# Performance work log

Measured on AMD Instinct MI355X. Metric: run time of the kernel, lower is better.

The kernel has to match this reference:

```python
import jax, jax.numpy as jnp
import numpy as np

N_LAT, N_LON = 121, 240
N = N_LAT * N_LON          # 29040 nodes (fixed by module's reshape)
DEG = 16
E = N * DEG                # 464640 edges
H = 128                    # input_nf = output_nf = hidden_nf
LV = 11                    # pressure levels (coord_mlp outputs 11*2)
EDGE_IN = 2 * H + 34       # source + target + w_diff(33) + edge_attr(1)


def setup_inputs() -> dict:
    key = jax.random.key(0)
    ks = jax.random.split(key, 18)
    def w(k, shape, s=0.05):
        return jax.random.normal(k, shape, dtype=jnp.float32) * s
    return {
        'h': w(ks[0], (N, H), 1.0),
        'u': w(ks[1], (N, LV), 1.0),
        'v': w(ks[2], (N, LV), 1.0),
        'edge_attr': w(ks[3], (E, 1), 1.0),
        # edge MLP: Linear(EDGE_IN,H) ReLU Linear(H,H) ReLU
        'W_e1': w(ks[4], (EDGE_IN, H)), 'b_e1': jnp.zeros((H,), jnp.float32),
        'W_e2': w(ks[5], (H, H)),       'b_e2': jnp.zeros((H,), jnp.float32),
        # node MLP: Linear(2H+H,H) ReLU Linear(H,H)
        'W_n1': w(ks[6], (3 * H, H)),   'b_n1': jnp.zeros((H,), jnp.float32),
        'W_n2': w(ks[7], (H, H)),       'b_n2': jnp.zeros((H,), jnp.float32),
        # coord MLP: Linear(H,H) ReLU Linear(H,22,bias=False) with tiny xavier gain
        'W_c1': w(ks[8], (H, H)),       'b_c1': jnp.zeros((H,), jnp.float32),
        'W_cl': w(ks[9], (H, 2 * LV), 0.001),
        'edge_index': jax.random.randint(ks[10], (2, E), 0, N, dtype=jnp.int32),
    }


def reference(h, u, v, edge_attr,
              W_e1, b_e1, W_e2, b_e2,
              W_n1, b_n1, W_n2, b_n2,
              W_c1, b_c1, W_cl,
              edge_index):
    row, col = edge_index[0], edge_index[1]

    # ---- coord2radial ----
    uc, vc = u[col], v[col]          # [E, LV]
    ur, vr = u[row], v[row]
    col_speed = jnp.sqrt(uc * uc + vc * vc)
    row_speed = jnp.sqrt(ur * ur + vr * vr)
    rel_dirt = (uc * ur + vc * vr) / (col_speed * row_speed)
    w_diff = jnp.concatenate([rel_dirt, col_speed, row_speed], axis=1)  # [E, 33]

    # ---- edge model ----
    edge_in = jnp.concatenate([h[row], h[col], w_diff, edge_attr], axis=1)  # [E, EDGE_IN]
    edge_feat = jax.nn.relu(jax.nn.relu(edge_in @ W_e1 + b_e1) @ W_e2 + b_e2)  # [E, H]

    # ---- node model (scatter-sum + lat-band mean pooling) ----
    agg = jax.ops.segment_sum(edge_feat, row, num_segments=N)  # [N, H]
    lat = agg.reshape(N_LAT, N_LON, H).mean(axis=1, keepdims=True)  # [121,1,H]
    lat_agg = jnp.broadcast_to(lat, (N_LAT, N_LON, H)).reshape(N, H)
    node_in = jnp.concatenate([h, agg, lat_agg], axis=1)  # [N, 3H]
    h_out = jax.nn.relu(node_in @ W_n1 + b_n1) @ W_n2 + b_n2 + h  # residual

    # ---- coord model (scatter-mean with clamp) ----
    ef = (jax.nn.relu(edge_feat @ W_c1 + b_c1) @ W_cl).reshape(E, 2, LV)
    radial = jnp.stack([uc, vc], axis=1)                 # [E, 2, LV]
    rad2 = jnp.sqrt(jnp.sum(radial * radial, axis=-1))   # [E, 2] (per-component magnitude)
    wind = ef * rad2[:, :, None]                         # [E, 2, LV]
    cnt = jnp.maximum(
        jax.ops.segment_sum(jnp.ones((E,), jnp.float32), row, num_segments=N), 1.0)[:, None]
    agg_u = jnp.clip(jax.ops.segment_sum(wind[:, 0, :], row, num_segments=N) / cnt, -100.0, 100.0)
    agg_v = jnp.clip(jax.ops.segment_sum(wind[:, 1, :], row, num_segments=N) / cnt, -100.0, 100.0)

    return h_out, agg_u, agg_v
```

## Files before the change

### kernel.cpp

```cpp
#include <hip/hip_runtime.h>
#include <hip/hip_bf16.h>
#include <math.h>

#define NN   29040
#define NLAT 121
#define NLON 240
#define HD   128
#define LVN  11
#define EE   464640

typedef __attribute__((ext_vector_type(8))) short short8;
typedef __attribute__((ext_vector_type(4))) float f4;

#define OFF_WE1 0
#define OFF_WE2 40960
#define OFF_WC1 57344
#define OFF_WCL 73728
#define OFF_WN1 77824
#define OFF_WN2 126976
#define WP_SHORTS 143360

__device__ inline short f2b(float x) {
    union { __hip_bfloat16 b; short s; } v;
    v.b = __float2bfloat16(x);
    return v.s;
}
__device__ inline float b2f(unsigned short b) {
    union { unsigned u; float f; } v; v.u = ((unsigned)b) << 16;
    return v.f;
}

#define SB_HIST  1815
#define SB_HCAST 1815
#define SB_UV    114
#define SB_WP    70

__global__ __launch_bounds__(256)
void setup_kernel(const int* __restrict__ eidx, int* __restrict__ cnt,
                  const float* __restrict__ h, short* __restrict__ hb,
                  const float* __restrict__ u, const float* __restrict__ v,
                  float* __restrict__ uvrec,
                  const float* __restrict__ We1, const float* __restrict__ We2,
                  const float* __restrict__ Wc1, const float* __restrict__ Wcl,
                  const float* __restrict__ Wn1, const float* __restrict__ Wn2,
                  short* __restrict__ wp)
{
    const int b = blockIdx.x, tid = threadIdx.x;
    if (b < SB_HIST) {
        int e = b * 256 + tid;
        atomicAdd(&cnt[eidx[e]], 1);
        return;
    }
    if (b < SB_HIST + SB_HCAST) {
        int idx = (b - SB_HIST) * 256 + tid;
        const float4* hf = (const float4*)h;
        float4 a = hf[idx * 2], c = hf[idx * 2 + 1];
        short8 o;
        o[0] = f2b(a.x); o[1] = f2b(a.y); o[2] = f2b(a.z); o[3] = f2b(a.w);
        o[4] = f2b(c.x); o[5] = f2b(c.y); o[6] = f2b(c.z); o[7] = f2b(c.w);
        ((short8*)hb)[idx] = o;
        return;
    }
    if (b < SB_HIST + SB_HCAST + SB_UV) {
        int n = (b - SB_HIST - SB_HCAST) * 256 + tid;
        if (n >= NN) return;
        float* r = uvrec + (size_t)n * 36;
        float un = 0.f, vn = 0.f;
#pragma unroll
        for (int l = 0; l < LVN; ++l) {
            float uu = u[n * LVN + l], vv = v[n * LVN + l];
            float s = sqrtf(uu * uu + vv * vv);
            r[l]      = uu / s;
            r[11 + l] = vv / s;
            r[22 + l] = s;
            un += uu * uu; vn += vv * vv;
        }
        r[33] = sqrtf(un);
        r[34] = sqrtf(vn);
        r[35] = 0.f;
        return;
    }
    {
        int fg = (b - SB_HIST - SB_HCAST - SB_UV) * 4 + (tid >> 6);
        const int l = tid & 63;
        int kind, f, base;
        if (fg < 80)       { kind = 0; f = fg;       base = OFF_WE1; }
        else if (fg < 112) { kind = 1; f = fg - 80;  base = OFF_WE2; }
        else if (fg < 144) { kind = 2; f = fg - 112; base = OFF_WC1; }
        else if (fg < 152) { kind = 3; f = fg - 144; base = OFF_WCL; }
        else if (fg < 248) { kind = 4; f = fg - 152; base = OFF_WN1; }
        else               { kind = 5; f = fg - 248; base = OFF_WN2; }
        const int nfw = (kind == 3) ? 2 : 8;
        const int kf = f / nfw, nf = f % nfw;
        short* dst = wp + base + (size_t)f * 512 + l * 8;
        for (int i = 0; i < 8; ++i) {
            int k = kf * 32 + ((l >> 4) << 3) + i;
            int n = nf * 16 + (l & 15);
            float val = 0.f;
            if (kind == 0) {
                int r = (k < 33) ? (256 + k) : (k == 33 ? 289 : (k < 64 ? -1 : k - 64));
                if (r >= 0) val = We1[r * HD + n];
            } else if (kind == 1) val = We2[k * HD + n];
            else if (kind == 2)  val = Wc1[k * HD + n];
            else if (kind == 3)  { if (n < 22) val = Wcl[k * 22 + n]; }
            else if (kind == 4)  val = Wn1[k * HD + n];
            else                 val = Wn2[k * HD + n];
            dst[i] = f2b(val);
        }
    }
}

__global__ __launch_bounds__(1024)
void scan_kernel(const int* __restrict__ cnt, int* __restrict__ off)
{
    __shared__ int part[1024];
    const int tid = threadIdx.x;
    const int CH = 29;
    int lo = tid * CH, hi = min(lo + CH, NN);
    int s = 0;
    for (int i = lo; i < hi; ++i) s += cnt[i];
    part[tid] = s;
    __syncthreads();
    for (int d = 1; d < 1024; d <<= 1) {
        int vv = (tid >= d) ? part[tid - d] : 0;
        __syncthreads();
        part[tid] += vv;
        __syncthreads();
    }
    int run = (tid == 0) ? 0 : part[tid - 1];
    for (int i = lo; i < hi; ++i) { off[i] = run; run += cnt[i]; }
    if (tid == 1023) off[NN] = run;
}

__global__ __launch_bounds__(256)
void scatter_kernel(const int* __restrict__ eidx, const int* __restrict__ off,
                    int* __restrict__ cur, int* __restrict__ csr)
{
    int e = blockIdx.x * 256 + threadIdx.x;
    if (e >= EE) return;
    int row = eidx[e];
    int p = atomicAdd(&cur[row], 1);
    csr[off[row] + p] = e;
}

template<int KF, int NF>
__device__ inline void layer_gemm(const short* At, int rs, const short* Wp,
                                  const float* bias, f4* acc, int w, int lane)
{
    const int m = 16 * w + (lane & 15);
    const char* arow = (const char*)At + m * rs;
    const int sw = (m & 7) << 4;
    const int kb = (lane >> 4) << 4;
#pragma unroll
    for (int nf = 0; nf < NF; ++nf) {
        float bv = bias ? bias[nf * 16 + (lane & 15)] : 0.f;
        acc[nf] = (f4){bv, bv, bv, bv};
    }
#pragma unroll
    for (int kf = 0; kf < KF; ++kf) {
        short8 a = *(const short8*)(arow + ((kf * 64 + kb) ^ sw));
        const short8* wr = (const short8*)(Wp + (size_t)kf * NF * 512) + lane;
#pragma unroll
        for (int nf = 0; nf < NF; ++nf) {
            short8 bfr = wr[nf * 64];
            acc[nf] = __builtin_amdgcn_mfma_f32_16x16x32_bf16(a, bfr, acc[nf], 0, 0, 0);
        }
    }
}

template<int NF>
__device__ inline void store_tile(short* tile, int rs, const f4* acc, int w, int lane)
{
    const int rb = 16 * w + ((lane >> 4) << 2);
    const int cb = (lane & 15) * 2;
#pragma unroll
    for (int nf = 0; nf < NF; ++nf)
#pragma unroll
        for (int r = 0; r < 4; ++r) {
            int row = rb + r;
            float vv = fmaxf(acc[nf][r], 0.f);
            *(short*)((char*)tile + row * rs + ((cb + nf * 32) ^ ((row & 7) << 4))) = f2b(vv);
        }
}

__global__ __launch_bounds__(256, 4)
void edge_mfma(const short* __restrict__ hb, const float* __restrict__ uvrec,
               const float* __restrict__ ea,
               const float* __restrict__ be1, const float* __restrict__ be2,
               const float* __restrict__ bc1,
               const short* __restrict__ wp,
               const int* __restrict__ eidx, const int* __restrict__ csr,
               float* __restrict__ agg, float* __restrict__ aggu,
               float* __restrict__ aggv)
{
    __shared__ short Twd[64 * 64];
    __shared__ short T1[64 * 128];
    __shared__ int   rows_s[64];
    __shared__ float radu_s[64], radv_s[64];

    const int tid = threadIdx.x, lane = tid & 63, w = tid >> 6;
    const int e0 = blockIdx.x * 64;
    const int mrow = 16 * w + (lane & 15);
    const int koff = 8 * (lane >> 4);
    const int sw   = (mrow & 7) << 4;

    int e1 = csr[e0 + mrow];
    int rowm = eidx[e1], colm = eidx[EE + e1];
    short8 ar[4], ac[4];
    {
        const short* hr = hb + (size_t)rowm * HD + koff;
        const short* hc = hb + (size_t)colm * HD + koff;
#pragma unroll
        for (int kf = 0; kf < 4; ++kf) {
            ar[kf] = *(const short8*)(hr + kf * 32);
            ac[kf] = *(const short8*)(hc + kf * 32);
        }
    }

    {
        const int m2 = tid >> 2, q = tid & 3;
        const int sw2 = (m2 & 7) << 4;
        int e2 = csr[e0 + m2];
        int row2 = eidx[e2], col2 = eidx[EE + e2];
        const float* rc = uvrec + (size_t)col2 * 36;
        const float* rr = uvrec + (size_t)row2 * 36;
        char* arow = (char*)(Twd + m2 * 64);
        short8 z = {0, 0, 0, 0, 0, 0, 0, 0};
        *(short8*)(arow + q * 32) = z;
        *(short8*)(arow + q * 32 + 16) = z;
        for (int l = q; l < LVN; l += 4) {
            float rel = rc[l] * rr[l] + rc[11 + l] * rr[11 + l];
            *(short*)(arow + ((2 * l) ^ sw2))        = f2b(rel);
            *(short*)(arow + ((2 * (11 + l)) ^ sw2)) = f2b(rc[22 + l]);
            *(short*)(arow + ((2 * (22 + l)) ^ sw2)) = f2b(rr[22 + l]);
        }
        if (q == 0) { rows_s[m2] = row2; radu_s[m2] = rc[33]; radv_s[m2] = rc[34]; }
        if (q == 3) *(short*)(arow + ((2 * 33) ^ sw2)) = f2b(ea[e2]);
    }
    __syncthreads();

    f4 acc[8];
#pragma unroll
    for (int nf = 0; nf < 8; ++nf) {
        float bv = be1[nf * 16 + (lane & 15)];
        acc[nf] = (f4){bv, bv, bv, bv};
    }
    {
        const char* awd = (const char*)(Twd + mrow * 64);
#pragma unroll
        for (int kf = 0; kf < 2; ++kf) {
            short8 a = *(const short8*)(awd + ((kf * 64 + 2 * koff) ^ sw));
            const short8* wr = (const short8*)(wp + OFF_WE1 + (size_t)kf * 8 * 512) + lane;
#pragma unroll
            for (int nf = 0; nf < 8; ++nf)
                acc[nf] = __builtin_amdgcn_mfma_f32_16x16x32_bf16(a, wr[nf * 64], acc[nf], 0, 0, 0);
        }
#pragma unroll
        for (int kf = 0; kf < 4; ++kf) {
            const short8* wr = (const short8*)(wp + OFF_WE1 + (size_t)(kf + 2) * 8 * 512) + lane;
#pragma unroll
            for (int nf = 0; nf < 8; ++nf)
                acc[nf] = __builtin_amdgcn_mfma_f32_16x16x32_bf16(ar[kf], wr[nf * 64], acc[nf], 0, 0, 0);
        }
#pragma unroll
        for (int kf = 0; kf < 4; ++kf) {
            const short8* wr = (const short8*)(wp + OFF_WE1 + (size_t)(kf + 6) * 8 * 512) + lane;
#pragma unroll
            for (int nf = 0; nf < 8; ++nf)
                acc[nf] = __builtin_amdgcn_mfma_f32_16x16x32_bf16(ac[kf], wr[nf * 64], acc[nf], 0, 0, 0);
        }
    }
    store_tile<8>(T1, 256, acc, w, lane);

    layer_gemm<4, 8>(T1, 256, wp + OFF_WE2, be2, acc, w, lane);
    store_tile<8>(T1, 256, acc, w, lane);

    f4 accC[8];
    layer_gemm<4, 8>(T1, 256, wp + OFF_WC1, bc1, accC, w, lane);

    __syncthreads();
    {
        const int n = tid & 127, qq = tid >> 7;
        const int m0 = qq * 32;
        int curr = rows_s[m0]; float s = 0.f;
        for (int m = m0; m < m0 + 32; ++m) {
            int r = rows_s[m];
            float vv = b2f(*(const unsigned short*)((const char*)(T1 + m * 128) + ((2 * n) ^ ((m & 7) << 4))));
            if (r != curr) { atomicAdd(&agg[(size_t)curr * HD + n], s); s = 0.f; curr = r; }
            s += vv;
        }
        atomicAdd(&agg[(size_t)curr * HD + n], s);
    }
    __syncthreads();

    store_tile<8>(T1, 256, accC, w, lane);
    layer_gemm<4, 2>(T1, 256, wp + OFF_WCL, (const float*)nullptr, accC, w, lane);
    float* O22 = (float*)Twd;
    {
        const int rb = 16 * w + ((lane >> 4) << 2), cb = lane & 15;
#pragma unroll
        for (int nf = 0; nf < 2; ++nf)
#pragma unroll
            for (int r = 0; r < 4; ++r)
                O22[(rb + r) * 32 + nf * 16 + cb] = accC[nf][r];
    }
    __syncthreads();

    {
        const int c = tid & 31, qq = tid >> 5;
        if (c < 22) {
            const bool isU = c < LVN;
            const int lvl = isU ? c : c - LVN;
            float* dst = isU ? aggu : aggv;
            const float* radp = isU ? radu_s : radv_s;
            const int m0 = qq * 8;
            int curr = rows_s[m0]; float s = 0.f;
            for (int m = m0; m < m0 + 8; ++m) {
                int r = rows_s[m];
                float vv = O22[m * 32 + c] * radp[m];
                if (r != curr) { atomicAdd(&dst[(size_t)curr * LVN + lvl], s); s = 0.f; curr = r; }
                s += vv;
            }
            atomicAdd(&dst[(size_t)curr * LVN + lvl], s);
        }
    }
}

__global__ __launch_bounds__(256)
void post_kernel(const float* __restrict__ agg, short* __restrict__ latb,
                 float* __restrict__ aggu, float* __restrict__ aggv,
                 const int* __restrict__ off)
{
    const int b = blockIdx.x, tid = threadIdx.x;
    if (b < NLAT) {
        __shared__ float part[256];
        const int j = tid & 127, half = tid >> 7;
        float s = 0.f;
        for (int lon = half * 120; lon < (half + 1) * 120; ++lon)
            s += agg[((size_t)b * NLON + lon) * HD + j];
        part[tid] = s;
        __syncthreads();
        if (tid < 128)
            latb[(size_t)b * HD + tid] = f2b((part[tid] + part[128 + tid]) * (1.0f / NLON));
        return;
    }
    int tt = (b - NLAT) * 256 + tid;
    if (tt >= NN * LVN) return;
    int n = tt / LVN;
    float c = fmaxf((float)(off[n + 1] - off[n]), 1.f);
    float xu = aggu[tt] / c, xv = aggv[tt] / c;
    aggu[tt] = fminf(fmaxf(xu, -100.f), 100.f);
    aggv[tt] = fminf(fmaxf(xv, -100.f), 100.f);
}

__global__ __launch_bounds__(512, 4)
void node_mfma(const short* __restrict__ hb, const float* __restrict__ h,
               const short* __restrict__ latb,
               const float* __restrict__ bn1, const float* __restrict__ bn2,
               const short* __restrict__ wp, float* __restrict__ out)
{
    __shared__ short T1[128 * 128];
    const int tid = threadIdx.x, lane = tid & 63, w = tid >> 6;
    const int n0 = blockIdx.x * 128;
    const int mrow = 16 * w + (lane & 15);
    const int koff = 8 * (lane >> 4);
    const int n = n0 + mrow;
    const int nc = (n < NN) ? n : (NN - 1);
    const short* hp = hb + (size_t)nc * HD + koff;
    const float* ap = out + (size_t)nc * HD + koff;
    const short* lp = latb + (size_t)(nc / NLON) * HD + koff;

    f4 acc[8];
#pragma unroll
    for (int nf = 0; nf < 8; ++nf) {
        float bv = bn1[nf * 16 + (lane & 15)];
        acc[nf] = (f4){bv, bv, bv, bv};
    }
#pragma unroll
    for (int kf = 0; kf < 4; ++kf) {
        short8 a = *(const short8*)(hp + kf * 32);
        const short8* wr = (const short8*)(wp + OFF_WN1 + (size_t)kf * 8 * 512) + lane;
#pragma unroll
        for (int nf = 0; nf < 8; ++nf)
            acc[nf] = __builtin_amdgcn_mfma_f32_16x16x32_bf16(a, wr[nf * 64], acc[nf], 0, 0, 0);
    }
#pragma unroll
    for (int kf = 0; kf < 4; ++kf) {
        short8 a;
#pragma unroll
        for (int j = 0; j < 8; ++j) a[j] = f2b(ap[kf * 32 + j]);
        const short8* wr = (const short8*)(wp + OFF_WN1 + (size_t)(kf + 4) * 8 * 512) + lane;
#pragma unroll
        for (int nf = 0; nf < 8; ++nf)
            acc[nf] = __builtin_amdgcn_mfma_f32_16x16x32_bf16(a, wr[nf * 64], acc[nf], 0, 0, 0);
    }
#pragma unroll
    for (int kf = 0; kf < 4; ++kf) {
        short8 a = *(const short8*)(lp + kf * 32);
        const short8* wr = (const short8*)(wp + OFF_WN1 + (size_t)(kf + 8) * 8 * 512) + lane;
#pragma unroll
        for (int nf = 0; nf < 8; ++nf)
            acc[nf] = __builtin_amdgcn_mfma_f32_16x16x32_bf16(a, wr[nf * 64], acc[nf], 0, 0, 0);
    }
    store_tile<8>(T1, 256, acc, w, lane);
    layer_gemm<4, 8>(T1, 256, wp + OFF_WN2, bn2, acc, w, lane);

    const int rb = 16 * w + ((lane >> 4) << 2), cb = lane & 15;
#pragma unroll
    for (int nf = 0; nf < 8; ++nf)
#pragma unroll
        for (int r = 0; r < 4; ++r) {
            int gn = n0 + rb + r;
            if (gn < NN) {
                int colj = nf * 16 + cb;
                out[(size_t)gn * HD + colj] = acc[nf][r] + h[(size_t)gn * HD + colj];
            }
        }
}

extern "C" void kernel_launch(void* const* d_in, const int* in_sizes, int n_in,
                              void* d_out, int out_size, void* d_ws, size_t ws_size,
                              hipStream_t stream)
{
    const float* h   = (const float*)d_in[0];
    const float* u   = (const float*)d_in[1];
    const float* v   = (const float*)d_in[2];
    const float* ea  = (const float*)d_in[3];
    const float* We1 = (const float*)d_in[4];
    const float* be1 = (const float*)d_in[5];
    const float* We2 = (const float*)d_in[6];
    const float* be2 = (const float*)d_in[7];
    const float* Wn1 = (const float*)d_in[8];
    const float* bn1 = (const float*)d_in[9];
    const float* Wn2 = (const float*)d_in[10];
    const float* bn2 = (const float*)d_in[11];
    const float* Wc1 = (const float*)d_in[12];
    const float* bc1 = (const float*)d_in[13];
    const float* Wcl = (const float*)d_in[14];
    const int*   eidx = (const int*)d_in[15];

    float* out  = (float*)d_out;
    float* agg  = out;
    float* aggu = out + (size_t)NN * HD;
    float* aggv = aggu + (size_t)NN * LVN;

    char* p = (char*)d_ws;
    short* wp  = (short*)p;                  p += (size_t)WP_SHORTS * 2;
    int*   off = (int*)p;                    p += (size_t)(NN + 1) * 4;
    int*   csr = (int*)p;                    p += (size_t)EE * 4;
    p = (char*)(((size_t)p + 15) & ~(size_t)15);
    short* hb  = (short*)p;                  p += (size_t)NN * HD * 2;
    float* uvr = (float*)p;                  p += (size_t)NN * 36 * 4;
    short* latb = (short*)p;                 p += (size_t)NLAT * HD * 2;
    p = (char*)(((size_t)p + 15) & ~(size_t)15);
    int*   cnt = (int*)p;                    p += (size_t)NN * 4;
    int*   cur = (int*)p;

    hipMemsetAsync(d_out, 0, (size_t)out_size * sizeof(float), stream);
    hipMemsetAsync(cnt, 0, (size_t)2 * NN * sizeof(int), stream);

    setup_kernel<<<SB_HIST + SB_HCAST + SB_UV + SB_WP, 256, 0, stream>>>(
        eidx, cnt, h, hb, u, v, uvr, We1, We2, Wc1, Wcl, Wn1, Wn2, wp);
    scan_kernel<<<1, 1024, 0, stream>>>(cnt, off);
    scatter_kernel<<<EE / 256, 256, 0, stream>>>(eidx, off, cur, csr);

    edge_mfma<<<EE / 64, 256, 0, stream>>>(hb, uvr, ea, be1, be2, bc1,
                                           wp, eidx, csr, agg, aggu, aggv);

    post_kernel<<<NLAT + (NN * LVN + 255) / 256, 256, 0, stream>>>(
        agg, latb, aggu, aggv, off);

    node_mfma<<<(NN + 127) / 128, 512, 0, stream>>>(hb, h, latb, bn1, bn2, wp, agg);
}
```

Baseline: 345.0 us.

## Switch edge and node MLPs to 32x32x16 MFMA with 2x2 wave tiling

Replaces the 16x16x32 bf16 MFMA tiling, where each wave owned 16 rows and all 128 columns, with 32x32x16 MFMA tiles. Waves are now arranged as row-groups by column-halves, so each wave computes a 32x64 sub-tile. Packed weights are re-laid out for the new B-fragment shape. Gathered h rows are loaded per k-step instead of being prefetched into registers, and extra __syncthreads are added because waves now share LDS tiles across column halves. The intent is higher MFMA efficiency and fewer weight loads per output. In exchange the coord-head GEMM runs on only half the waves, and the added barriers and unprefetched gathers may stall.

Result: faster. 294.6 us (-14.6%).

```diff
diff --git a/kernel.cpp b/kernel.cpp
--- a/kernel.cpp
+++ b/kernel.cpp
@@ -10,7 +10,7 @@
 #define EE   464640
 
 typedef __attribute__((ext_vector_type(8))) short short8;
-typedef __attribute__((ext_vector_type(4))) float f4;
+typedef __attribute__((ext_vector_type(16))) float f16v;
 
 #define OFF_WE1 0
 #define OFF_WE2 40960
@@ -90,12 +90,12 @@
         else if (fg < 152) { kind = 3; f = fg - 144; base = OFF_WCL; }
         else if (fg < 248) { kind = 4; f = fg - 152; base = OFF_WN1; }
         else               { kind = 5; f = fg - 248; base = OFF_WN2; }
-        const int nfw = (kind == 3) ? 2 : 8;
+        const int nfw = (kind == 3) ? 1 : 4;
         const int kf = f / nfw, nf = f % nfw;
         short* dst = wp + base + (size_t)f * 512 + l * 8;
         for (int i = 0; i < 8; ++i) {
-            int k = kf * 32 + ((l >> 4) << 3) + i;
-            int n = nf * 16 + (l & 15);
+            int k = kf * 16 + ((l >> 5) << 3) + i;
+            int n = nf * 32 + (l & 31);
             float val = 0.f;
             if (kind == 0) {
                 int r = (k < 33) ? (256 + k) : (k == 33 ? 289 : (k < 64 ? -1 : k - 64));
@@ -143,43 +143,43 @@
     csr[off[row] + p] = e;
 }
 
-template<int KF, int NF>
-__device__ inline void layer_gemm(const short* At, int rs, const short* Wp,
-                                  const float* bias, f4* acc, int w, int lane)
-{
-    const int m = 16 * w + (lane & 15);
-    const char* arow = (const char*)At + m * rs;
-    const int sw = (m & 7) << 4;
-    const int kb = (lane >> 4) << 4;
-#pragma unroll
-    for (int nf = 0; nf < NF; ++nf) {
-        float bv = bias ? bias[nf * 16 + (lane & 15)] : 0.f;
-        acc[nf] = (f4){bv, bv, bv, bv};
+template<int KF, int NFL, int NJ>
+__device__ inline void gemm32_lds(const short* At, const short* Wp, int nf0,
+                                  const float* bias, f16v* acc,
+                                  int mrow, int colbase, int r31, int kh, int lane)
+{
+    const char* arow = (const char*)At + mrow * 256;
+    const int sw = (mrow & 7) << 4;
+#pragma unroll
+    for (int j = 0; j < NJ; ++j) {
+        float bv = bias ? bias[colbase + j * 32 + r31] : 0.f;
+#pragma unroll
+        for (int q = 0; q < 16; ++q) acc[j][q] = bv;
     }
 #pragma unroll
     for (int kf = 0; kf < KF; ++kf) {
-        short8 a = *(const short8*)(arow + ((kf * 64 + kb) ^ sw));
-        const short8* wr = (const short8*)(Wp + (size_t)kf * NF * 512) + lane;
-#pragma unroll
-        for (int nf = 0; nf < NF; ++nf) {
-            short8 bfr = wr[nf * 64];
-            acc[nf] = __builtin_amdgcn_mfma_f32_16x16x32_bf16(a, bfr, acc[nf], 0, 0, 0);
-        }
-    }
-}
-
-template<int NF>
-__device__ inline void store_tile(short* tile, int rs, const f4* acc, int w, int lane)
-{
-    const int rb = 16 * w + ((lane >> 4) << 2);
-    const int cb = (lane & 15) * 2;
-#pragma unroll
-    for (int nf = 0; nf < NF; ++nf)
-#pragma unroll
-        for (int r = 0; r < 4; ++r) {
-            int row = rb + r;
-            float vv = fmaxf(acc[nf][r], 0.f);
-            *(short*)((char*)tile + row * rs + ((cb + nf * 32) ^ ((row & 7) << 4))) = f2b(vv);
+        short8 a = *(const short8*)(arow + ((kf * 32 + 16 * kh) ^ sw));
+#pragma unroll
+        for (int j = 0; j < NJ; ++j) {
+            short8 bfr = *(const short8*)(Wp + (size_t)(kf * NFL + nf0 + j) * 512 + lane * 8);
+            acc[j] = __builtin_amdgcn_mfma_f32_32x32x16_bf16(a, bfr, acc[j], 0, 0, 0);
+        }
+    }
+}
+
+template<int NJ>
+__device__ inline void store32(short* tile, const f16v* acc, int rg, int colbase,
+                               int r31, int kh, bool relu)
+{
+#pragma unroll
+    for (int j = 0; j < NJ; ++j)
+#pragma unroll
+        for (int reg = 0; reg < 16; ++reg) {
+            int row = rg * 32 + (reg & 3) + 8 * (reg >> 2) + 4 * kh;
+            int cb2 = (colbase + j * 32 + r31) * 2;
+            float vv = acc[j][reg];
+            if (relu) vv = fmaxf(vv, 0.f);
+            *(short*)((char*)tile + row * 256 + (cb2 ^ ((row & 7) << 4))) = f2b(vv);
         }
 }
 
@@ -199,23 +199,17 @@
     __shared__ float radu_s[64], radv_s[64];
 
     const int tid = threadIdx.x, lane = tid & 63, w = tid >> 6;
+    const int rg = w >> 1, cg = w & 1;
     const int e0 = blockIdx.x * 64;
-    const int mrow = 16 * w + (lane & 15);
-    const int koff = 8 * (lane >> 4);
-    const int sw   = (mrow & 7) << 4;
+    const int r31 = lane & 31, kh = lane >> 5;
+    const int mrow = rg * 32 + r31;
+    const int sw = (mrow & 7) << 4;
+    const int colbase = cg * 64;
 
     int e1 = csr[e0 + mrow];
     int rowm = eidx[e1], colm = eidx[EE + e1];
-    short8 ar[4], ac[4];
-    {
-        const short* hr = hb + (size_t)rowm * HD + koff;
-        const short* hc = hb + (size_t)colm * HD + koff;
-#pragma unroll
-        for (int kf = 0; kf < 4; ++kf) {
-            ar[kf] = *(const short8*)(hr + kf * 32);
-            ac[kf] = *(const short8*)(hc + kf * 32);
-        }
-    }
+    const short* hr = hb + (size_t)rowm * HD + 8 * kh;
+    const short* hc = hb + (size_t)colm * HD + 8 * kh;
 
     {
         const int m2 = tid >> 2, q = tid & 3;
@@ -239,83 +233,87 @@
     }
     __syncthreads();
 
-    f4 acc[8];
-#pragma unroll
-    for (int nf = 0; nf < 8; ++nf) {
-        float bv = be1[nf * 16 + (lane & 15)];
-        acc[nf] = (f4){bv, bv, bv, bv};
+    f16v acc[2];
+#pragma unroll
+    for (int j = 0; j < 2; ++j) {
+        float bv = be1[colbase + j * 32 + r31];
+#pragma unroll
+        for (int q = 0; q < 16; ++q) acc[j][q] = bv;
     }
     {
         const char* awd = (const char*)(Twd + mrow * 64);
 #pragma unroll
-        for (int kf = 0; kf < 2; ++kf) {
-            short8 a = *(const short8*)(awd + ((kf * 64 + 2 * koff) ^ sw));
-            const short8* wr = (const short8*)(wp + OFF_WE1 + (size_t)kf * 8 * 512) + lane;
-#pragma unroll
-            for (int nf = 0; nf < 8; ++nf)
-                acc[nf] = __builtin_amdgcn_mfma_f32_16x16x32_bf16(a, wr[nf * 64], acc[nf], 0, 0, 0);
-        }
-#pragma unroll
         for (int kf = 0; kf < 4; ++kf) {
-            const short8* wr = (const short8*)(wp + OFF_WE1 + (size_t)(kf + 2) * 8 * 512) + lane;
-#pragma unroll
-            for (int nf = 0; nf < 8; ++nf)
-                acc[nf] = __builtin_amdgcn_mfma_f32_16x16x32_bf16(ar[kf], wr[nf * 64], acc[nf], 0, 0, 0);
-        }
-#pragma unroll
-        for (int kf = 0; kf < 4; ++kf) {
-            const short8* wr = (const short8*)(wp + OFF_WE1 + (size_t)(kf + 6) * 8 * 512) + lane;
-#pragma unroll
-            for (int nf = 0; nf < 8; ++nf)
-                acc[nf] = __builtin_amdgcn_mfma_f32_16x16x32_bf16(ac[kf], wr[nf * 64], acc[nf], 0, 0, 0);
-        }
-    }
-    store_tile<8>(T1, 256, acc, w, lane);
-
-    layer_gemm<4, 8>(T1, 256, wp + OFF_WE2, be2, acc, w, lane);
-    store_tile<8>(T1, 256, acc, w, lane);
-
-    f4 accC[8];
-    layer_gemm<4, 8>(T1, 256, wp + OFF_WC1, bc1, accC, w, lane);
-
-    __syncthreads();
+            short8 a = *(const short8*)(awd + ((kf * 32 + 16 * kh) ^ sw));
+#pragma unroll
+            for (int j = 0; j < 2; ++j) {
+                short8 bfr = *(const short8*)(wp + OFF_WE1 + (size_t)(kf * 4 + cg * 2 + j) * 512 + lane * 8);
+                acc[j] = __builtin_amdgcn_mfma_f32_32x32x16_bf16(a, bfr, acc[j], 0, 0, 0);
+            }
+        }
+#pragma unroll
+        for (int s = 0; s < 8; ++s) {
+            short8 a = *(const short8*)(hr + s * 16);
+#pragma unroll
+            for (int j = 0; j < 2; ++j) {
+                short8 bfr = *(const short8*)(wp + OFF_WE1 + (size_t)((s + 4) * 4 + cg * 2 + j) * 512 + lane * 8);
+                acc[j] = __builtin_amdgcn_mfma_f32_32x32x16_bf16(a, bfr, acc[j], 0, 0, 0);
+            }
+        }
+#pragma unroll
+        for (int s = 0; s < 8; ++s) {
+            short8 a = *(const short8*)(hc + s * 16);
+#pragma unroll
+            for (int j = 0; j < 2; ++j) {
+                short8 bfr = *(const short8*)(wp + OFF_WE1 + (size_t)((s + 12) * 4 + cg * 2 + j) * 512 + lane * 8);
+                acc[j] = __builtin_amdgcn_mfma_f32_32x32x16_bf16(a, bfr, acc[j], 0, 0, 0);
+            }
+        }
+    }
+    store32<2>(T1, acc, rg, colbase, r31, kh, true);
+    __syncthreads();
+
+    gemm32_lds<8, 4, 2>(T1, wp + OFF_WE2, cg * 2, be2, acc, mrow, colbase, r31, kh, lane);
+    __syncthreads();
+    store32<2>(T1, acc, rg, colbase, r31, kh, true);
+    __syncthreads();
+
+    gemm32_lds<8, 4, 2>(T1, wp + OFF_WC1, cg * 2, bc1, acc, mrow, colbase, r31, kh, lane);
+
     {
-        const int n = tid & 127, qq = tid >> 7;
-        const int m0 = qq * 32;
-        int curr = rows_s[m0]; float s = 0.f;
+        const int col = colbase + lane;
+        const int m0 = rg * 32;
+        int curr = rows_s[m0];
+        float s = 0.f;
         for (int m = m0; m < m0 + 32; ++m) {
             int r = rows_s[m];
-            float vv = b2f(*(const unsigned short*)((const char*)(T1 + m * 128) + ((2 * n) ^ ((m & 7) << 4))));
-            if (r != curr) { atomicAdd(&agg[(size_t)curr * HD + n], s); s = 0.f; curr = r; }
+            float vv = b2f(*(const unsigned short*)((const char*)T1 + m * 256 + (((col & 127) * 2) ^ ((m & 7) << 4))));
+            if (r != curr) { atomicAdd(&agg[(size_t)curr * HD + (col & 127)], s); s = 0.f; curr = r; }
             s += vv;
         }
-        atomicAdd(&agg[(size_t)curr * HD + n], s);
-    }
-    __syncthreads();
-
-    store_tile<8>(T1, 256, accC, w, lane);
-    layer_gemm<4, 2>(T1, 256, wp + OFF_WCL, (const float*)nullptr, accC, w, lane);
-    float* O22 = (float*)Twd;
-    {
-        const int rb = 16 * w + ((lane >> 4) << 2), cb = lane & 15;
-#pragma unroll
-        for (int nf = 0; nf < 2; ++nf)
-#pragma unroll
-            for (int r = 0; r < 4; ++r)
-                O22[(rb + r) * 32 + nf * 16 + cb] = accC[nf][r];
-    }
-    __syncthreads();
-
-    {
-        const int c = tid & 31, qq = tid >> 5;
+        atomicAdd(&agg[(size_t)curr * HD + (col & 127)], s);
+    }
+    __syncthreads();
+    store32<2>(T1, acc, rg, colbase, r31, kh, true);
+    __syncthreads();
+
+    if (cg == 0) {
+        gemm32_lds<8, 1, 1>(T1, wp + OFF_WCL, 0, (const float*)nullptr, acc, mrow, 0, r31, kh, lane);
+        float* O22 = (float*)Twd;
+#pragma unroll
+        for (int reg = 0; reg < 16; ++reg) {
+            int row = rg * 32 + (reg & 3) + 8 * (reg >> 2) + 4 * kh;
+            O22[row * 32 + r31] = acc[0][reg];
+        }
+        const int c = r31;
         if (c < 22) {
             const bool isU = c < LVN;
             const int lvl = isU ? c : c - LVN;
             float* dst = isU ? aggu : aggv;
             const float* radp = isU ? radu_s : radv_s;
-            const int m0 = qq * 8;
+            const int m0 = rg * 32 + kh * 16;
             int curr = rows_s[m0]; float s = 0.f;
-            for (int m = m0; m < m0 + 8; ++m) {
+            for (int m = m0; m < m0 + 16; ++m) {
                 int r = rows_s[m];
                 float vv = O22[m * 32 + c] * radp[m];
                 if (r != curr) { atomicAdd(&dst[(size_t)curr * LVN + lvl], s); s = 0.f; curr = r; }
@@ -361,59 +359,66 @@
 {
     __shared__ short T1[128 * 128];
     const int tid = threadIdx.x, lane = tid & 63, w = tid >> 6;
+    const int rg = w >> 1, cg = w & 1;
+    const int r31 = lane & 31, kh = lane >> 5;
+    const int mrow = rg * 32 + r31;
+    const int colbase = cg * 64;
     const int n0 = blockIdx.x * 128;
-    const int mrow = 16 * w + (lane & 15);
-    const int koff = 8 * (lane >> 4);
     const int n = n0 + mrow;
     const int nc = (n < NN) ? n : (NN - 1);
-    const short* hp = hb + (size_t)nc * HD + koff;
-    const float* ap = out + (size_t)nc * HD + koff;
-    const short* lp = latb + (size_t)(nc / NLON) * HD + koff;
-
-    f4 acc[8];
-#pragma unroll
-    for (int nf = 0; nf < 8; ++nf) {
-        float bv = bn1[nf * 16 + (lane & 15)];
-        acc[nf] = (f4){bv, bv, bv, bv};
-    }
-#pragma unroll
-    for (int kf = 0; kf < 4; ++kf) {
-        short8 a = *(const short8*)(hp + kf * 32);
-        const short8* wr = (const short8*)(wp + OFF_WN1 + (size_t)kf * 8 * 512) + lane;
-#pragma unroll
-        for (int nf = 0; nf < 8; ++nf)
-            acc[nf] = __builtin_amdgcn_mfma_f32_16x16x32_bf16(a, wr[nf * 64], acc[nf], 0, 0, 0);
-    }
-#pragma unroll
-    for (int kf = 0; kf < 4; ++kf) {
+    const short* hp = hb + (size_t)nc * HD + 8 * kh;
+    const float* ap = out + (size_t)nc * HD + 8 * kh;
+    const short* lp = latb + (size_t)(nc / NLON) * HD + 8 * kh;
+
+    f16v acc[2];
+#pragma unroll
+    for (int j = 0; j < 2; ++j) {
+        float bv = bn1[colbase + j * 32 + r31];
+#pragma unroll
+        for (int q = 0; q < 16; ++q) acc[j][q] = bv;
+    }
+#pragma unroll
+    for (int s = 0; s < 8; ++s) {
+        short8 a = *(const short8*)(hp + s * 16);
+#pragma unroll
+        for (int j = 0; j < 2; ++j) {
+            short8 bfr = *(const short8*)(wp + OFF_WN1 + (size_t)(s * 4 + cg * 2 + j) * 512 + lane * 8);
+            acc[j] = __builtin_amdgcn_mfma_f32_32x32x16_bf16(a, bfr, acc[j], 0, 0, 0);
+        }
+    }
+#pragma unroll
+    for (int s = 0; s < 8; ++s) {
         short8 a;
 #pragma unroll
-        for (int j = 0; j < 8; ++j) a[j] = f2b(ap[kf * 32 + j]);
-        const short8* wr = (const short8*)(wp + OFF_WN1 + (size_t)(kf + 4) * 8 * 512) + lane;
-#pragma unroll
-        for (int nf = 0; nf < 8; ++nf)
-            acc[nf] = __builtin_amdgcn_mfma_f32_16x16x32_bf16(a, wr[nf * 64], acc[nf], 0, 0, 0);
-    }
-#pragma unroll
-    for (int kf = 0; kf < 4; ++kf) {
-        short8 a = *(const short8*)(lp + kf * 32);
-        const short8* wr = (const short8*)(wp + OFF_WN1 + (size_t)(kf + 8) * 8 * 512) + lane;
-#pragma unroll
-        for (int nf = 0; nf < 8; ++nf)
-            acc[nf] = __builtin_amdgcn_mfma_f32_16x16x32_bf16(a, wr[nf * 64], acc[nf], 0, 0, 0);
-    }
-    store_tile<8>(T1, 256, acc, w, lane);
-    layer_gemm<4, 8>(T1, 256, wp + OFF_WN2, bn2, acc, w, lane);
-
-    const int rb = 16 * w + ((lane >> 4) << 2), cb = lane & 15;
-#pragma unroll
-    for (int nf = 0; nf < 8; ++nf)
-#pragma unroll
-        for (int r = 0; r < 4; ++r) {
-            int gn = n0 + rb + r;
+        for (int q = 0; q < 8; ++q) a[q] = f2b(ap[s * 16 + q]);
+#pragma unroll
+        for (int j = 0; j < 2; ++j) {
+            short8 bfr = *(const short8*)(wp + OFF_WN1 + (size_t)((s + 8) * 4 + cg * 2 + j) * 512 + lane * 8);
+            acc[j] = __builtin_amdgcn_mfma_f32_32x32x16_bf16(a, bfr, acc[j], 0, 0, 0);
+        }
+    }
+#pragma unroll
+    for (int s = 0; s < 8; ++s) {
+        short8 a = *(const short8*)(lp + s * 16);
+#pragma unroll
+        for (int j = 0; j < 2; ++j) {
+            short8 bfr = *(const short8*)(wp + OFF_WN1 + (size_t)((s + 16) * 4 + cg * 2 + j) * 512 + lane * 8);
+            acc[j] = __builtin_amdgcn_mfma_f32_32x32x16_bf16(a, bfr, acc[j], 0, 0, 0);
+        }
+    }
+    store32<2>(T1, acc, rg, colbase, r31, kh, true);
+    __syncthreads();
+    gemm32_lds<8, 4, 2>(T1, wp + OFF_WN2, cg * 2, bn2, acc, mrow, colbase, r31, kh, lane);
+
+#pragma unroll
+    for (int j = 0; j < 2; ++j)
+#pragma unroll
+        for (int reg = 0; reg < 16; ++reg) {
+            int row = rg * 32 + (reg & 3) + 8 * (reg >> 2) + 4 * kh;
+            int gn = n0 + row;
             if (gn < NN) {
-                int colj = nf * 16 + cb;
-                out[(size_t)gn * HD + colj] = acc[nf][r] + h[(size_t)gn * HD + colj];
+                int col = colbase + j * 32 + r31;
+                out[(size_t)gn * HD + col] = acc[j][reg] + h[(size_t)gn * HD + col];
             }
         }
 }
```
